# Performance work log

Hardware: AMD Instinct MI355X
Metric: run time of the kernel (lower is better)

## Reference

```python
import jax, jax.numpy as jnp
import numpy as np

N_NODES = 100000
N_EDGES = 3200000
D_IN = 256
D_OUT = 256


def setup_inputs() -> dict:
    key = jax.random.key(0)
    k1, k2, k3, k4, k5, k6 = jax.random.split(key, 6)
    x = jax.random.normal(k1, (N_NODES, D_IN), dtype=jnp.float32)
    edge_src = jax.random.randint(k2, (N_EDGES,), 0, N_NODES, dtype=jnp.int64)
    edge_dst = jax.random.randint(k3, (N_EDGES,), 0, N_NODES, dtype=jnp.int64)
    adj_vals = jax.random.uniform(k4, (N_EDGES,), dtype=jnp.float32)
    # xavier_uniform with gain=2.0: bound = gain * sqrt(6/(fan_in+fan_out))
    bound = 2.0 * np.sqrt(6.0 / (D_IN + D_OUT))
    w_nbr = jax.random.uniform(k5, (D_IN, D_OUT), dtype=jnp.float32, minval=-bound, maxval=bound)
    w_own = jax.random.uniform(k6, (D_IN, D_OUT), dtype=jnp.float32, minval=-bound, maxval=bound)
    bias = jnp.zeros((D_OUT,), dtype=jnp.float32)
    return {"x": x, "edge_src": edge_src, "edge_dst": edge_dst, "adj_vals": adj_vals,
            "w_nbr": w_nbr, "w_own": w_own, "bias": bias}


def reference(x, edge_src, edge_dst, adj_vals, w_nbr, w_own, bias):
    # h = x @ W_nbr  (transform first, then sparse aggregate: adj @ h)
    h = x @ w_nbr                                   # [N, D_out]
    msgs = adj_vals[:, None] * h[edge_src]          # [E, D_out]
    agg = jax.ops.segment_sum(msgs, edge_dst, num_segments=x.shape[0])  # [N, D_out]
    return agg + x @ w_own + bias
```

## Files before the change

### kernel.cpp

```cpp
#include <hip/hip_runtime.h>
#include <hip/hip_fp16.h>

#define DN 256
#define KTOT 512
#define GBM 128
#define GBK 64

typedef __attribute__((ext_vector_type(8))) short bf16x8;
typedef __attribute__((ext_vector_type(8))) unsigned short u16x8;
typedef __attribute__((ext_vector_type(4))) float f32x4;

__device__ __forceinline__ unsigned short f2b(float f) {
    unsigned u = __float_as_uint(f);
    u += 0x7FFF + ((u >> 16) & 1);
    return (unsigned short)(u >> 16);
}
__device__ __forceinline__ float b2f(unsigned short b) {
    return __uint_as_float(((unsigned)b) << 16);
}


__global__ void k_hist(const int* __restrict__ dst, int* __restrict__ deg, int E) {
    int e = blockIdx.x * blockDim.x + threadIdx.x;
    if (e < E) atomicAdd(&deg[dst[e]], 1);
}

__global__ void k_block_sums(const int* __restrict__ deg, int* __restrict__ bsum, int N) {
    __shared__ int s[256];
    int t = threadIdx.x;
    int base = blockIdx.x * 1024 + t * 4;
    int sum = 0;
#pragma unroll
    for (int j = 0; j < 4; ++j) {
        int i = base + j;
        if (i < N) sum += deg[i];
    }
    s[t] = sum;
    __syncthreads();
    for (int off = 128; off > 0; off >>= 1) {
        if (t < off) s[t] += s[t + off];
        __syncthreads();
    }
    if (t == 0) bsum[blockIdx.x] = s[0];
}

__global__ void k_scan_bsums(const int* __restrict__ bsum, int* __restrict__ boffs, int NB) {
    __shared__ int s[128];
    int t = threadIdx.x;
    int v = (t < NB) ? bsum[t] : 0;
    s[t] = v;
    __syncthreads();
    for (int off = 1; off < 128; off <<= 1) {
        int u = (t >= off) ? s[t - off] : 0;
        __syncthreads();
        s[t] += u;
        __syncthreads();
    }
    if (t < NB) boffs[t] = s[t] - v;
}

__global__ void k_scan_final(const int* __restrict__ deg, const int* __restrict__ boffs,
                             int* __restrict__ row_ptr, int* __restrict__ cursor,
                             int N, int E) {
    __shared__ int s[256];
    int t = threadIdx.x;
    int base = blockIdx.x * 1024 + t * 4;
    int d[4];
    int sum = 0;
#pragma unroll
    for (int j = 0; j < 4; ++j) {
        int i = base + j;
        d[j] = (i < N) ? deg[i] : 0;
        sum += d[j];
    }
    s[t] = sum;
    __syncthreads();
    for (int off = 1; off < 256; off <<= 1) {
        int u = (t >= off) ? s[t - off] : 0;
        __syncthreads();
        s[t] += u;
        __syncthreads();
    }
    int p = boffs[blockIdx.x] + s[t] - sum;
#pragma unroll
    for (int j = 0; j < 4; ++j) {
        int i = base + j;
        if (i < N) {
            row_ptr[i] = p;
            cursor[i]  = p;
            p += d[j];
        }
    }
    if (blockIdx.x == 0 && t == 0) row_ptr[N] = E;
}

__global__ void k_scatter(const int* __restrict__ src, const int* __restrict__ dst,
                          const float* __restrict__ vals, int* __restrict__ cursor,
                          long long* __restrict__ csr, int E) {
    int e = blockIdx.x * blockDim.x + threadIdx.x;
    if (e < E) {
        int d = dst[e];
        int pos = atomicAdd(&cursor[d], 1);
        long long packed = (long long)(unsigned)src[e] |
                           ((long long)__float_as_int(vals[e]) << 32);
        csr[pos] = packed;
    }
}


__global__ void k_cvt_x(const float* __restrict__ x, __half* __restrict__ xh, int total8) {
    int t = blockIdx.x * blockDim.x + threadIdx.x;
    if (t >= total8) return;
    const float4* p = (const float4*)(x + (size_t)t * 8);
    float4 a = p[0], b = p[1];
    __half h[8];
    h[0] = __float2half(a.x); h[1] = __float2half(a.y);
    h[2] = __float2half(a.z); h[3] = __float2half(a.w);
    h[4] = __float2half(b.x); h[5] = __float2half(b.y);
    h[6] = __float2half(b.z); h[7] = __float2half(b.w);
    *(u16x8*)(xh + (size_t)t * 8) = *(const u16x8*)h;
}

__global__ void k_cvt_w(const float* __restrict__ wn, const float* __restrict__ wo,
                        unsigned short* __restrict__ wth, unsigned short* __restrict__ wtl) {
    int t = blockIdx.x * blockDim.x + threadIdx.x;
    int k = t >> 8;
    int n = t & 255;
    float v = (k < 256) ? wn[k * 256 + n] : wo[(k - 256) * 256 + n];
    unsigned short h = f2b(v);
    unsigned short l = f2b(v - b2f(h));
    wth[(size_t)n * KTOT + k] = h;
    wtl[(size_t)n * KTOT + k] = l;
}


__global__ void k_agg_f16(const __half* __restrict__ xh, const int* __restrict__ row_ptr,
                          const long long* __restrict__ csr, float* __restrict__ out, int N) {
    int lane = threadIdx.x & 63;
    int n = blockIdx.x * 4 + (threadIdx.x >> 6);
    if (n >= N) return;
    int beg = row_ptr[n], end = row_ptr[n + 1];
    float ax = 0.f, ay = 0.f, az = 0.f, aw = 0.f;
    int i = beg;
    for (; i + 4 <= end; i += 4) {
        long long e0 = csr[i], e1 = csr[i + 1], e2 = csr[i + 2], e3 = csr[i + 3];
        const __half2* p0 = (const __half2*)(xh + (size_t)(int)e0 * DN) + lane * 2;
        const __half2* p1 = (const __half2*)(xh + (size_t)(int)e1 * DN) + lane * 2;
        const __half2* p2 = (const __half2*)(xh + (size_t)(int)e2 * DN) + lane * 2;
        const __half2* p3 = (const __half2*)(xh + (size_t)(int)e3 * DN) + lane * 2;
        __half2 a0 = p0[0], b0 = p0[1];
        __half2 a1 = p1[0], b1 = p1[1];
        __half2 a2 = p2[0], b2 = p2[1];
        __half2 a3 = p3[0], b3 = p3[1];
        float v0 = __int_as_float((int)(e0 >> 32));
        float v1 = __int_as_float((int)(e1 >> 32));
        float v2 = __int_as_float((int)(e2 >> 32));
        float v3 = __int_as_float((int)(e3 >> 32));
        ax = fmaf(v0, __half2float(a0.x), ax); ay = fmaf(v0, __half2float(a0.y), ay);
        az = fmaf(v0, __half2float(b0.x), az); aw = fmaf(v0, __half2float(b0.y), aw);
        ax = fmaf(v1, __half2float(a1.x), ax); ay = fmaf(v1, __half2float(a1.y), ay);
        az = fmaf(v1, __half2float(b1.x), az); aw = fmaf(v1, __half2float(b1.y), aw);
        ax = fmaf(v2, __half2float(a2.x), ax); ay = fmaf(v2, __half2float(a2.y), ay);
        az = fmaf(v2, __half2float(b2.x), az); aw = fmaf(v2, __half2float(b2.y), aw);
        ax = fmaf(v3, __half2float(a3.x), ax); ay = fmaf(v3, __half2float(a3.y), ay);
        az = fmaf(v3, __half2float(b3.x), az); aw = fmaf(v3, __half2float(b3.y), aw);
    }
    for (; i < end; ++i) {
        long long e0 = csr[i];
        const __half2* p0 = (const __half2*)(xh + (size_t)(int)e0 * DN) + lane * 2;
        __half2 a0 = p0[0], b0 = p0[1];
        float v0 = __int_as_float((int)(e0 >> 32));
        ax = fmaf(v0, __half2float(a0.x), ax); ay = fmaf(v0, __half2float(a0.y), ay);
        az = fmaf(v0, __half2float(b0.x), az); aw = fmaf(v0, __half2float(b0.y), aw);
    }
    float4 o = make_float4(ax, ay, az, aw);
    ((float4*)(out + (size_t)n * DN))[lane] = o;
}

__global__ void k_agg_f32(const float* __restrict__ x, const int* __restrict__ row_ptr,
                          const long long* __restrict__ csr, float* __restrict__ out, int N) {
    int lane = threadIdx.x & 63;
    int n = blockIdx.x * 4 + (threadIdx.x >> 6);
    if (n >= N) return;
    int beg = row_ptr[n], end = row_ptr[n + 1];
    float4 acc = make_float4(0.f, 0.f, 0.f, 0.f);
    int i = beg;
    for (; i + 2 <= end; i += 2) {
        long long e0 = csr[i], e1 = csr[i + 1];
        float4 a = ((const float4*)(x + (size_t)(int)e0 * DN))[lane];
        float4 b = ((const float4*)(x + (size_t)(int)e1 * DN))[lane];
        float v0 = __int_as_float((int)(e0 >> 32));
        float v1 = __int_as_float((int)(e1 >> 32));
        acc.x = fmaf(v0, a.x, acc.x); acc.y = fmaf(v0, a.y, acc.y);
        acc.z = fmaf(v0, a.z, acc.z); acc.w = fmaf(v0, a.w, acc.w);
        acc.x = fmaf(v1, b.x, acc.x); acc.y = fmaf(v1, b.y, acc.y);
        acc.z = fmaf(v1, b.z, acc.z); acc.w = fmaf(v1, b.w, acc.w);
    }
    if (i < end) {
        long long e0 = csr[i];
        float4 a = ((const float4*)(x + (size_t)(int)e0 * DN))[lane];
        float v0 = __int_as_float((int)(e0 >> 32));
        acc.x = fmaf(v0, a.x, acc.x); acc.y = fmaf(v0, a.y, acc.y);
        acc.z = fmaf(v0, a.z, acc.z); acc.w = fmaf(v0, a.w, acc.w);
    }
    ((float4*)(out + (size_t)n * DN))[lane] = acc;
}


__device__ __forceinline__ void cvt8(const float4 a, const float4 b, u16x8& h, u16x8& lo) {
    float f[8] = {a.x, a.y, a.z, a.w, b.x, b.y, b.z, b.w};
#pragma unroll
    for (int j = 0; j < 8; ++j) {
        unsigned short hb = f2b(f[j]);
        h[j] = hb;
        lo[j] = f2b(f[j] - b2f(hb));
    }
}

__global__ __launch_bounds__(512) void k_gemm(const float* __restrict__ x,
                                              const unsigned short* __restrict__ wth,
                                              const unsigned short* __restrict__ wtl,
                                              const float* __restrict__ bias,
                                              float* __restrict__ out, int N) {
    __shared__ unsigned short Ah[GBM * GBK];
    __shared__ unsigned short Al[GBM * GBK];

    int t = threadIdx.x;
    int l = t & 63;
    int wid = t >> 6;
    int wr = wid >> 2;
    int wc = wid & 3;
    int r0 = blockIdx.x * GBM;
    int lr = l & 15;
    int lg = l >> 4;

    f32x4 acc[4][4];
#pragma unroll
    for (int m = 0; m < 4; ++m)
#pragma unroll
        for (int n = 0; n < 4; ++n) acc[m][n] = (f32x4)(0.f);

    int srow = t >> 2;
    int sseg = t & 3;

#pragma unroll 1
    for (int c = 0; c < 8; ++c) {
        int k0 = c * GBK;
        const float* src = (k0 < 256) ? out : x;
        int kc = k0 & 255;
        __syncthreads();
        {
            int grow = r0 + srow;
            if (grow >= N) grow = N - 1;
            const float4* p = (const float4*)(src + (size_t)grow * DN + kc + sseg * 16);
            float4 v0 = p[0], v1 = p[1], v2 = p[2], v3 = p[3];
            u16x8 h0, l0, h1, l1;
            cvt8(v0, v1, h0, l0);
            cvt8(v2, v3, h1, l1);
            int kg0 = sseg * 2, kg1 = sseg * 2 + 1;
            int rb = srow * 128;
            int sw = (srow & 7) << 4;
            *(u16x8*)((char*)Ah + rb + (((kg0 << 4)) ^ sw)) = h0;
            *(u16x8*)((char*)Al + rb + (((kg0 << 4)) ^ sw)) = l0;
            *(u16x8*)((char*)Ah + rb + (((kg1 << 4)) ^ sw)) = h1;
            *(u16x8*)((char*)Al + rb + (((kg1 << 4)) ^ sw)) = l1;
        }
        __syncthreads();
#pragma unroll
        for (int ks = 0; ks < 2; ++ks) {
            bf16x8 ah[4], al[4], bh[4], bl[4];
            int kg = ks * 4 + lg;
#pragma unroll
            for (int m = 0; m < 4; ++m) {
                int rl = wr * 64 + m * 16 + lr;
                int off = rl * 128 + (((kg << 4)) ^ ((rl & 7) << 4));
                ah[m] = *(const bf16x8*)((const char*)Ah + off);
                al[m] = *(const bf16x8*)((const char*)Al + off);
            }
#pragma unroll
            for (int n = 0; n < 4; ++n) {
                int col = wc * 64 + n * 16 + lr;
                size_t e = (size_t)col * KTOT + k0 + ks * 32 + lg * 8;
                bh[n] = *(const bf16x8*)(wth + e);
                bl[n] = *(const bf16x8*)(wtl + e);
            }
#pragma unroll
            for (int m = 0; m < 4; ++m)
#pragma unroll
                for (int n = 0; n < 4; ++n) {
                    acc[m][n] = __builtin_amdgcn_mfma_f32_16x16x32_bf16(ah[m], bh[n], acc[m][n], 0, 0, 0);
                    acc[m][n] = __builtin_amdgcn_mfma_f32_16x16x32_bf16(ah[m], bl[n], acc[m][n], 0, 0, 0);
                    acc[m][n] = __builtin_amdgcn_mfma_f32_16x16x32_bf16(al[m], bh[n], acc[m][n], 0, 0, 0);
                }
        }
    }

    float bv[4];
#pragma unroll
    for (int n = 0; n < 4; ++n) bv[n] = bias[wc * 64 + n * 16 + lr];

#pragma unroll
    for (int m = 0; m < 4; ++m) {
#pragma unroll
        for (int j = 0; j < 4; ++j) {
            int grow = r0 + wr * 64 + m * 16 + lg * 4 + j;
            if (grow < N) {
                float* orow = out + (size_t)grow * DN + wc * 64;
#pragma unroll
                for (int n = 0; n < 4; ++n) orow[n * 16 + lr] = acc[m][n][j] + bv[n];
            }
        }
    }
}


extern "C" void kernel_launch(void* const* d_in, const int* in_sizes, int n_in,
                              void* d_out, int out_size, void* d_ws, size_t ws_size,
                              hipStream_t stream) {
    const float* x    = (const float*)d_in[0];
    const int*   esrc = (const int*)d_in[1];
    const int*   edst = (const int*)d_in[2];
    const float* vals = (const float*)d_in[3];
    const float* wn   = (const float*)d_in[4];
    const float* wo   = (const float*)d_in[5];
    const float* bias = (const float*)d_in[6];
    float* out = (float*)d_out;

    int N = in_sizes[0] / DN;
    int E = in_sizes[1];

    char* ws = (char*)d_ws;
    size_t off = 0;
    auto alloc = [&](size_t bytes) { void* p = ws + off; off = (off + bytes + 255) & ~(size_t)255; return p; };

    int* deg      = (int*)alloc((size_t)N * 4);
    int* row_ptr  = (int*)alloc((size_t)(N + 1) * 4);
    int* cursor   = (int*)alloc((size_t)N * 4);
    int* bsum     = (int*)alloc(512);
    int* boffs    = (int*)alloc(512);
    long long* csr = (long long*)alloc((size_t)E * 8);
    unsigned short* wth = (unsigned short*)alloc((size_t)DN * KTOT * 2);
    unsigned short* wtl = (unsigned short*)alloc((size_t)DN * KTOT * 2);
    size_t xh_bytes = (size_t)N * DN * 2;
    bool use_f16 = (off + xh_bytes) <= ws_size;
    __half* xh = use_f16 ? (__half*)alloc(xh_bytes) : nullptr;

    int NB = (N + 1023) / 1024;

    hipMemsetAsync(deg, 0, (size_t)N * 4, stream);
    k_cvt_w<<<(KTOT * DN) / 256, 256, 0, stream>>>(wn, wo, wth, wtl);
    if (use_f16) {
        int total8 = N * DN / 8;
        k_cvt_x<<<(total8 + 255) / 256, 256, 0, stream>>>(x, xh, total8);
    }
    k_hist<<<(E + 255) / 256, 256, 0, stream>>>(edst, deg, E);
    k_block_sums<<<NB, 256, 0, stream>>>(deg, bsum, N);
    k_scan_bsums<<<1, 128, 0, stream>>>(bsum, boffs, NB);
    k_scan_final<<<NB, 256, 0, stream>>>(deg, boffs, row_ptr, cursor, N, E);
    k_scatter<<<(E + 255) / 256, 256, 0, stream>>>(esrc, edst, vals, cursor, csr, E);
    if (use_f16)
        k_agg_f16<<<(N + 3) / 4, 256, 0, stream>>>(xh, row_ptr, csr, out, N);
    else
        k_agg_f32<<<(N + 3) / 4, 256, 0, stream>>>(x, row_ptr, csr, out, N);
    k_gemm<<<(N + GBM - 1) / GBM, 512, 0, stream>>>(x, wth, wtl, bias, out, N);
}
```

Measured before the change: 976.3 us.

## Replace per-node CSR with bucketed partitioned sort and per-bucket aggregation

Replaces the per-node CSR build with a coarse bucket sort: edges are grouped into buckets of 32 destination nodes, with 8 partitions per bucket keyed by block index to spread atomic contention. The destination offset within the bucket is packed into the edge record. A new aggregation kernel loads each bucket's edges into LDS. Each wave scans the whole bucket, keeps only edges whose nodes it owns, and accumulates into an 8-entry register array. The aim is to shrink the histogram/scan size and make the scatter writes more local. The trade-offs are that every wave reads every edge in its bucket, the accumulator array is indexed dynamically (which may cause register indexing or spills), and each iteration issues only one gather, so fewer loads are in flight.

```diff
diff --git a/kernel.cpp b/kernel.cpp
--- a/kernel.cpp
+++ b/kernel.cpp
@@ -5,6 +5,9 @@
 #define KTOT 512
 #define GBM 128
 #define GBK 64
+#define BKT_NODES 32
+#define NPART 8
+#define LDS_CAP 4096
 
 typedef __attribute__((ext_vector_type(8))) short bf16x8;
 typedef __attribute__((ext_vector_type(8))) unsigned short u16x8;
@@ -20,12 +23,25 @@
 }
 
 
-__global__ void k_hist(const int* __restrict__ dst, int* __restrict__ deg, int E) {
-    int e = blockIdx.x * blockDim.x + threadIdx.x;
-    if (e < E) atomicAdd(&deg[dst[e]], 1);
-}
-
-__global__ void k_block_sums(const int* __restrict__ deg, int* __restrict__ bsum, int N) {
+__global__ void k_bhist(const int* __restrict__ edst, int* __restrict__ hist, int E) {
+    int e = blockIdx.x * 256 + threadIdx.x;
+    if (e < E) atomicAdd(&hist[(edst[e] >> 5) * NPART + (blockIdx.x & 7)], 1);
+}
+
+__global__ void k_bscatter(const int* __restrict__ esrc, const int* __restrict__ edst,
+                           const float* __restrict__ vals, int* __restrict__ cursor,
+                           long long* __restrict__ mid, int E) {
+    int e = blockIdx.x * 256 + threadIdx.x;
+    if (e < E) {
+        int d = edst[e];
+        int pos = atomicAdd(&cursor[(d >> 5) * NPART + (blockIdx.x & 7)], 1);
+        unsigned lo = (unsigned)esrc[e] | ((unsigned)(d & 31) << 20);
+        mid[pos] = (long long)lo | ((long long)(unsigned)__float_as_int(vals[e]) << 32);
+    }
+}
+
+
+__global__ void k_block_sums(const int* __restrict__ v, int* __restrict__ bsum, int L) {
     __shared__ int s[256];
     int t = threadIdx.x;
     int base = blockIdx.x * 1024 + t * 4;
@@ -33,7 +49,7 @@
 #pragma unroll
     for (int j = 0; j < 4; ++j) {
         int i = base + j;
-        if (i < N) sum += deg[i];
+        if (i < L) sum += v[i];
     }
     s[t] = sum;
     __syncthreads();
@@ -59,9 +75,9 @@
     if (t < NB) boffs[t] = s[t] - v;
 }
 
-__global__ void k_scan_final(const int* __restrict__ deg, const int* __restrict__ boffs,
-                             int* __restrict__ row_ptr, int* __restrict__ cursor,
-                             int N, int E) {
+__global__ void k_scan_final(const int* __restrict__ v, const int* __restrict__ boffs,
+                             int* __restrict__ offs, int* __restrict__ cursor,
+                             int L, int E) {
     __shared__ int s[256];
     int t = threadIdx.x;
     int base = blockIdx.x * 1024 + t * 4;
@@ -70,7 +86,7 @@
 #pragma unroll
     for (int j = 0; j < 4; ++j) {
         int i = base + j;
-        d[j] = (i < N) ? deg[i] : 0;
+        d[j] = (i < L) ? v[i] : 0;
         sum += d[j];
     }
     s[t] = sum;
@@ -85,26 +101,13 @@
 #pragma unroll
     for (int j = 0; j < 4; ++j) {
         int i = base + j;
-        if (i < N) {
-            row_ptr[i] = p;
-            cursor[i]  = p;
+        if (i < L) {
+            offs[i]   = p;
+            cursor[i] = p;
             p += d[j];
         }
     }
-    if (blockIdx.x == 0 && t == 0) row_ptr[N] = E;
-}
-
-__global__ void k_scatter(const int* __restrict__ src, const int* __restrict__ dst,
-                          const float* __restrict__ vals, int* __restrict__ cursor,
-                          long long* __restrict__ csr, int E) {
-    int e = blockIdx.x * blockDim.x + threadIdx.x;
-    if (e < E) {
-        int d = dst[e];
-        int pos = atomicAdd(&cursor[d], 1);
-        long long packed = (long long)(unsigned)src[e] |
-                           ((long long)__float_as_int(vals[e]) << 32);
-        csr[pos] = packed;
-    }
+    if (blockIdx.x == 0 && t == 0) offs[L] = E;
 }
 
 
@@ -134,76 +137,61 @@
 }
 
 
-__global__ void k_agg_f16(const __half* __restrict__ xh, const int* __restrict__ row_ptr,
-                          const long long* __restrict__ csr, float* __restrict__ out, int N) {
-    int lane = threadIdx.x & 63;
-    int n = blockIdx.x * 4 + (threadIdx.x >> 6);
-    if (n >= N) return;
-    int beg = row_ptr[n], end = row_ptr[n + 1];
-    float ax = 0.f, ay = 0.f, az = 0.f, aw = 0.f;
-    int i = beg;
-    for (; i + 4 <= end; i += 4) {
-        long long e0 = csr[i], e1 = csr[i + 1], e2 = csr[i + 2], e3 = csr[i + 3];
-        const __half2* p0 = (const __half2*)(xh + (size_t)(int)e0 * DN) + lane * 2;
-        const __half2* p1 = (const __half2*)(xh + (size_t)(int)e1 * DN) + lane * 2;
-        const __half2* p2 = (const __half2*)(xh + (size_t)(int)e2 * DN) + lane * 2;
-        const __half2* p3 = (const __half2*)(xh + (size_t)(int)e3 * DN) + lane * 2;
-        __half2 a0 = p0[0], b0 = p0[1];
-        __half2 a1 = p1[0], b1 = p1[1];
-        __half2 a2 = p2[0], b2 = p2[1];
-        __half2 a3 = p3[0], b3 = p3[1];
-        float v0 = __int_as_float((int)(e0 >> 32));
-        float v1 = __int_as_float((int)(e1 >> 32));
-        float v2 = __int_as_float((int)(e2 >> 32));
-        float v3 = __int_as_float((int)(e3 >> 32));
-        ax = fmaf(v0, __half2float(a0.x), ax); ay = fmaf(v0, __half2float(a0.y), ay);
-        az = fmaf(v0, __half2float(b0.x), az); aw = fmaf(v0, __half2float(b0.y), aw);
-        ax = fmaf(v1, __half2float(a1.x), ax); ay = fmaf(v1, __half2float(a1.y), ay);
-        az = fmaf(v1, __half2float(b1.x), az); aw = fmaf(v1, __half2float(b1.y), aw);
-        ax = fmaf(v2, __half2float(a2.x), ax); ay = fmaf(v2, __half2float(a2.y), ay);
-        az = fmaf(v2, __half2float(b2.x), az); aw = fmaf(v2, __half2float(b2.y), aw);
-        ax = fmaf(v3, __half2float(a3.x), ax); ay = fmaf(v3, __half2float(a3.y), ay);
-        az = fmaf(v3, __half2float(b3.x), az); aw = fmaf(v3, __half2float(b3.y), aw);
-    }
-    for (; i < end; ++i) {
-        long long e0 = csr[i];
-        const __half2* p0 = (const __half2*)(xh + (size_t)(int)e0 * DN) + lane * 2;
-        __half2 a0 = p0[0], b0 = p0[1];
-        float v0 = __int_as_float((int)(e0 >> 32));
-        ax = fmaf(v0, __half2float(a0.x), ax); ay = fmaf(v0, __half2float(a0.y), ay);
-        az = fmaf(v0, __half2float(b0.x), az); aw = fmaf(v0, __half2float(b0.y), aw);
-    }
-    float4 o = make_float4(ax, ay, az, aw);
-    ((float4*)(out + (size_t)n * DN))[lane] = o;
-}
-
-__global__ void k_agg_f32(const float* __restrict__ x, const int* __restrict__ row_ptr,
-                          const long long* __restrict__ csr, float* __restrict__ out, int N) {
-    int lane = threadIdx.x & 63;
-    int n = blockIdx.x * 4 + (threadIdx.x >> 6);
-    if (n >= N) return;
-    int beg = row_ptr[n], end = row_ptr[n + 1];
-    float4 acc = make_float4(0.f, 0.f, 0.f, 0.f);
-    int i = beg;
-    for (; i + 2 <= end; i += 2) {
-        long long e0 = csr[i], e1 = csr[i + 1];
-        float4 a = ((const float4*)(x + (size_t)(int)e0 * DN))[lane];
-        float4 b = ((const float4*)(x + (size_t)(int)e1 * DN))[lane];
-        float v0 = __int_as_float((int)(e0 >> 32));
-        float v1 = __int_as_float((int)(e1 >> 32));
-        acc.x = fmaf(v0, a.x, acc.x); acc.y = fmaf(v0, a.y, acc.y);
-        acc.z = fmaf(v0, a.z, acc.z); acc.w = fmaf(v0, a.w, acc.w);
-        acc.x = fmaf(v1, b.x, acc.x); acc.y = fmaf(v1, b.y, acc.y);
-        acc.z = fmaf(v1, b.z, acc.z); acc.w = fmaf(v1, b.w, acc.w);
-    }
-    if (i < end) {
-        long long e0 = csr[i];
-        float4 a = ((const float4*)(x + (size_t)(int)e0 * DN))[lane];
-        float v0 = __int_as_float((int)(e0 >> 32));
-        acc.x = fmaf(v0, a.x, acc.x); acc.y = fmaf(v0, a.y, acc.y);
-        acc.z = fmaf(v0, a.z, acc.z); acc.w = fmaf(v0, a.w, acc.w);
-    }
-    ((float4*)(out + (size_t)n * DN))[lane] = acc;
+template<int USE_F16>
+__global__ __launch_bounds__(256) void k_agg_bkt(const __half* __restrict__ xh,
+                                                 const float* __restrict__ xf,
+                                                 const int* __restrict__ offs,
+                                                 const long long* __restrict__ mid,
+                                                 float* __restrict__ out, int N) {
+    __shared__ long long smid[LDS_CAP];
+    int k = blockIdx.x;
+    int t = threadIdx.x;
+    int lane = t & 63;
+    int wid = t >> 6;
+
+    int beg = offs[k * NPART];
+    int end = offs[k * NPART + NPART];
+    int cnt = end - beg;
+    int lcnt = cnt < LDS_CAP ? cnt : LDS_CAP;
+    for (int i = t; i < lcnt; i += 256) smid[i] = mid[beg + i];
+    __syncthreads();
+
+    float4 acc[8];
+#pragma unroll
+    for (int j = 0; j < 8; ++j) acc[j] = make_float4(0.f, 0.f, 0.f, 0.f);
+
+    for (int i = 0; i < cnt; ++i) {
+        long long e = (i < LDS_CAP) ? smid[i] : mid[beg + i];
+        unsigned lo = (unsigned)e;
+        int dlo = (lo >> 20) & 31;
+        if ((dlo & 3) != wid) continue;
+        int src = lo & 0xFFFFF;
+        float val = __int_as_float((int)(e >> 32));
+        int j = dlo >> 2;
+        if (USE_F16) {
+            float2 raw = *((const float2*)(xh + (size_t)src * DN) + lane);
+            __half2 h01 = *(__half2*)&raw.x;
+            __half2 h23 = *(__half2*)&raw.y;
+            float2 f01 = __half22float2(h01);
+            float2 f23 = __half22float2(h23);
+            acc[j].x = fmaf(val, f01.x, acc[j].x);
+            acc[j].y = fmaf(val, f01.y, acc[j].y);
+            acc[j].z = fmaf(val, f23.x, acc[j].z);
+            acc[j].w = fmaf(val, f23.y, acc[j].w);
+        } else {
+            float4 r = *((const float4*)(xf + (size_t)src * DN) + lane);
+            acc[j].x = fmaf(val, r.x, acc[j].x);
+            acc[j].y = fmaf(val, r.y, acc[j].y);
+            acc[j].z = fmaf(val, r.z, acc[j].z);
+            acc[j].w = fmaf(val, r.w, acc[j].w);
+        }
+    }
+
+#pragma unroll
+    for (int j = 0; j < 8; ++j) {
+        int node = k * BKT_NODES + j * 4 + wid;
+        if (node < N) ((float4*)(out + (size_t)node * DN))[lane] = acc[j];
+    }
 }
 
 
@@ -329,38 +317,42 @@
     int N = in_sizes[0] / DN;
     int E = in_sizes[1];
 
+    int NBKT = (N + BKT_NODES - 1) / BKT_NODES;
+    int L = NBKT * NPART;
+
     char* ws = (char*)d_ws;
     size_t off = 0;
     auto alloc = [&](size_t bytes) { void* p = ws + off; off = (off + bytes + 255) & ~(size_t)255; return p; };
 
-    int* deg      = (int*)alloc((size_t)N * 4);
-    int* row_ptr  = (int*)alloc((size_t)(N + 1) * 4);
-    int* cursor   = (int*)alloc((size_t)N * 4);
+    int* hist     = (int*)alloc((size_t)L * 4);
+    int* offs     = (int*)alloc((size_t)(L + 1) * 4);
+    int* cursor   = (int*)alloc((size_t)L * 4);
     int* bsum     = (int*)alloc(512);
     int* boffs    = (int*)alloc(512);
-    long long* csr = (long long*)alloc((size_t)E * 8);
+    long long* mid = (long long*)alloc((size_t)E * 8);
     unsigned short* wth = (unsigned short*)alloc((size_t)DN * KTOT * 2);
     unsigned short* wtl = (unsigned short*)alloc((size_t)DN * KTOT * 2);
     size_t xh_bytes = (size_t)N * DN * 2;
     bool use_f16 = (off + xh_bytes) <= ws_size;
     __half* xh = use_f16 ? (__half*)alloc(xh_bytes) : nullptr;
 
-    int NB = (N + 1023) / 1024;
-
-    hipMemsetAsync(deg, 0, (size_t)N * 4, stream);
+    int NB = (L + 1023) / 1024;
+    int EB = (E + 255) / 256;
+
+    hipMemsetAsync(hist, 0, (size_t)L * 4, stream);
     k_cvt_w<<<(KTOT * DN) / 256, 256, 0, stream>>>(wn, wo, wth, wtl);
     if (use_f16) {
         int total8 = N * DN / 8;
         k_cvt_x<<<(total8 + 255) / 256, 256, 0, stream>>>(x, xh, total8);
     }
-    k_hist<<<(E + 255) / 256, 256, 0, stream>>>(edst, deg, E);
-    k_block_sums<<<NB, 256, 0, stream>>>(deg, bsum, N);
+    k_bhist<<<EB, 256, 0, stream>>>(edst, hist, E);
+    k_block_sums<<<NB, 256, 0, stream>>>(hist, bsum, L);
     k_scan_bsums<<<1, 128, 0, stream>>>(bsum, boffs, NB);
-    k_scan_final<<<NB, 256, 0, stream>>>(deg, boffs, row_ptr, cursor, N, E);
-    k_scatter<<<(E + 255) / 256, 256, 0, stream>>>(esrc, edst, vals, cursor, csr, E);
+    k_scan_final<<<NB, 256, 0, stream>>>(hist, boffs, offs, cursor, L, E);
+    k_bscatter<<<EB, 256, 0, stream>>>(esrc, edst, vals, cursor, mid, E);
     if (use_f16)
-        k_agg_f16<<<(N + 3) / 4, 256, 0, stream>>>(xh, row_ptr, csr, out, N);
+        k_agg_bkt<1><<<NBKT, 256, 0, stream>>>(xh, x, offs, mid, out, N);
     else
-        k_agg_f32<<<(N + 3) / 4, 256, 0, stream>>>(x, row_ptr, csr, out, N);
+        k_agg_bkt<0><<<NBKT, 256, 0, stream>>>(xh, x, offs, mid, out, N);
     k_gemm<<<(N + GBM - 1) / GBM, 512, 0, stream>>>(x, wth, wtl, bias, out, N);
 }
```

Result: slower. 2.018 ms (+106.7%).
